# Performance work log

Hardware: AMD Instinct MI355X
Metric: run time of the kernel (lower is better)

The kernel has to match this reference:

```python
import jax, jax.numpy as jnp
import numpy as np

N, M, K, C = 2048, 2048, 32, 256
AW, NE, H, S = 32, 128, 8, 32
LMAX = 2
HID = min(128, AW // 2)          # 16, hidden width of radial MLPs
EC = AW + NE + C                 # 416, edge feature dim
M0 = 2 * AW * (LMAX + 1)         # 192, q/k degree-dot feature dim
SLICES = [(0, 1), (1, 4), (4, 9)]  # m-slices for l = 0, 1, 2


def _ln(x, g, b, eps=1e-5):
    mu = jnp.mean(x, -1, keepdims=True)
    var = jnp.mean(jnp.square(x - mu), -1, keepdims=True)
    return (x - mu) * jax.lax.rsqrt(var + eps) * g + b


def _radial(x, w1, b1, g1, be1, w2, b2, g2, be2, w3, b3):
    # EquiformerV2-style RadialFunction: Linear->LN->SiLU x2 -> Linear
    h = jax.nn.silu(_ln(x @ w1.T + b1, g1, be1))
    h = jax.nn.silu(_ln(h @ w2.T + b2, g2, be2))
    return h @ w3.T + b3


def _so3_linear(x, W, b):
    # per-degree channel mixing; bias only on l=0. x: [..., 9, Cin], W: [3, Cout, Cin]
    outs = []
    for l, (s, e) in enumerate(SLICES):
        o = jnp.einsum('...mc,dc->...md', x[..., s:e, :], W[l])
        if l == 0:
            o = o + b
        outs.append(o)
    return jnp.concatenate(outs, axis=-2)


def _sph_all(vec):
    # real spherical harmonics l=0..2 of normalized vec, integral normalization
    v = vec / (jnp.linalg.norm(vec, axis=-1, keepdims=True) + 1e-12)
    x, y, z = v[..., 0], v[..., 1], v[..., 2]
    y0 = jnp.full(x.shape, 0.28209479177387814)
    c1 = 0.4886025119029199
    c2a, c2b, c2c = 1.0925484305920792, 0.31539156525252005, 0.5462742152960396
    return jnp.stack([y0, c1 * y, c1 * z, c1 * x,
                      c2a * x * y, c2a * y * z, c2b * (3.0 * z * z - 1.0),
                      c2a * x * z, c2c * (x * x - y * y)], axis=-1)


def _smooth_leaky(x, a=0.2):
    return 0.5 * (1 + a) * x + 0.5 * (1 - a) * x * (2.0 * jax.nn.sigmoid(x) - 1.0)


def _forward(node_pos, node_irreps_input, edge_dis, edge_vec, attn_weight,
             cluster_irreps_input, tgt_emb, W_dot, b_dot,
             rm0_w1, rm0_b1, rm0_g1, rm0_be1, rm0_w2, rm0_b2, rm0_g2, rm0_be2, rm0_w3, rm0_b3,
             fc_m0_w, fc_m0_b, an_g, an_b, alpha_dot,
             rv_w1, rv_b1, rv_g1, rv_be1, rv_w2, rv_b2, rv_g2, rv_be2, rv_w3, rv_b3,
             wz, bz, atomic_numbers, attn_mask, f_sparse_idx_expnode):
    n, k = attn_weight.shape[0], attn_weight.shape[1]
    aw = jnp.where(attn_mask, 0.0, attn_weight)                 # mask padded neighbors
    tgt = tgt_emb[atomic_numbers]                               # [N,NE]
    idx = f_sparse_idx_expnode                                  # [N,K] cluster gather index
    cl_scal = cluster_irreps_input[:, 0, :][idx]                # [N,K,C] scalar (l=0) part
    x_edge = jnp.concatenate(
        [aw, jnp.broadcast_to(tgt[:, None, :], (n, k, tgt.shape[-1])), cl_scal], -1)

    # dot_alpha attention logits: per-degree <feat, Y_l(r_ij)> for query and gathered key
    q = _so3_linear(node_irreps_input, W_dot, b_dot)            # [N,9,AW]
    key = _so3_linear(cluster_irreps_input, W_dot, b_dot)[idx]  # [N,K,9,AW]
    sh = _sph_all(edge_vec)                                     # [N,K,9]
    dots = [jnp.einsum('nmc,nkm->nkc', q[:, s:e, :], sh[..., s:e]) for s, e in SLICES]
    dots += [jnp.einsum('nkmc,nkm->nkc', key[:, :, s:e, :], sh[..., s:e]) for s, e in SLICES]
    m0 = jnp.concatenate(dots, -1)                              # [N,K,M0]

    ew = _radial(x_edge, rm0_w1, rm0_b1, rm0_g1, rm0_be1, rm0_w2, rm0_b2, rm0_g2, rm0_be2, rm0_w3, rm0_b3)
    af = ((m0 * ew) @ fc_m0_w.T + fc_m0_b).reshape(n, k, H, S)
    af = _smooth_leaky(_ln(af, an_g, an_b))
    logits = jnp.einsum('nkhs,hs->nkh', af, alpha_dot)
    logits = jnp.where(attn_mask, -1e9, logits)
    alpha = jax.nn.softmax(logits, axis=1)                      # [N,K,H]

    # zero-order value path: radial edge weight modulates gathered equivariant values
    vw = _radial(x_edge, rv_w1, rv_b1, rv_g1, rv_be1, rv_w2, rv_b2, rv_g2, rv_be2, rv_w3, rv_b3)
    v = (cluster_irreps_input[idx] * vw[:, :, None, :]).reshape(n, k, 9, H, C // H)
    out = jnp.einsum('nkh,nkmhc->nmhc', alpha, v).reshape(n, 9, C)
    return _so3_linear(out, wz, bz)                             # [N,9,C]


def setup_inputs() -> dict:
    ks = iter(jax.random.split(jax.random.key(0), 64))
    nrm = lambda shape, s=1.0: jax.random.normal(next(ks), shape, jnp.float32) * s
    inp = {}
    inp['node_pos'] = nrm((N, 3))
    inp['node_irreps_input'] = nrm((N, 9, C))
    inp['edge_dis'] = jax.random.uniform(next(ks), (N, K), jnp.float32) * 5.0
    inp['edge_vec'] = nrm((N, K, 3))
    inp['attn_weight'] = nrm((N, K, AW))
    inp['atomic_numbers'] = jax.random.randint(next(ks), (N,), 0, 256)
    inp['attn_mask'] = jax.random.bernoulli(next(ks), 0.1, (N, K, 1))
    inp['f_sparse_idx_expnode'] = jax.random.randint(next(ks), (N, K), 0, M)
    inp['cluster_irreps_input'] = nrm((M, 9, C))
    inp['tgt_emb'] = jax.random.uniform(next(ks), (256, NE), jnp.float32, -0.001, 0.001)
    inp['W_dot'] = nrm((3, AW, C), C ** -0.5)
    inp['b_dot'] = jnp.zeros((AW,), jnp.float32)

    def rad_params(pfx, out_dim):
        d = {}
        d[pfx + '_w1'] = nrm((HID, EC), EC ** -0.5); d[pfx + '_b1'] = jnp.zeros((HID,), jnp.float32)
        d[pfx + '_g1'] = jnp.ones((HID,), jnp.float32); d[pfx + '_be1'] = jnp.zeros((HID,), jnp.float32)
        d[pfx + '_w2'] = nrm((HID, HID), HID ** -0.5); d[pfx + '_b2'] = jnp.zeros((HID,), jnp.float32)
        d[pfx + '_g2'] = jnp.ones((HID,), jnp.float32); d[pfx + '_be2'] = jnp.zeros((HID,), jnp.float32)
        d[pfx + '_w3'] = nrm((out_dim, HID), HID ** -0.5); d[pfx + '_b3'] = jnp.zeros((out_dim,), jnp.float32)
        return d

    inp.update(rad_params('rm0', M0))
    inp['fc_m0_w'] = nrm((H * S, M0), M0 ** -0.5)
    inp['fc_m0_b'] = jnp.zeros((H * S,), jnp.float32)
    inp['an_g'] = jnp.ones((S,), jnp.float32)
    inp['an_b'] = jnp.zeros((S,), jnp.float32)
    std = S ** -0.5
    inp['alpha_dot'] = jax.random.uniform(next(ks), (H, S), jnp.float32, -std, std)
    inp.update(rad_params('rv', C))
    inp['wz'] = nrm((3, C, C), C ** -0.5)
    inp['bz'] = jnp.zeros((C,), jnp.float32)
    return inp


def reference(node_pos, node_irreps_input, edge_dis, edge_vec, attn_weight, atomic_numbers,
              attn_mask, f_sparse_idx_expnode, cluster_irreps_input, tgt_emb, W_dot, b_dot,
              rm0_w1, rm0_b1, rm0_g1, rm0_be1, rm0_w2, rm0_b2, rm0_g2, rm0_be2, rm0_w3, rm0_b3,
              fc_m0_w, fc_m0_b, an_g, an_b, alpha_dot,
              rv_w1, rv_b1, rv_g1, rv_be1, rv_w2, rv_b2, rv_g2, rv_be2, rv_w3, rv_b3,
              wz, bz):
    return _forward(node_pos, node_irreps_input, edge_dis, edge_vec, attn_weight,
                    cluster_irreps_input, tgt_emb, W_dot, b_dot,
                    rm0_w1, rm0_b1, rm0_g1, rm0_be1, rm0_w2, rm0_b2, rm0_g2, rm0_be2, rm0_w3, rm0_b3,
                    fc_m0_w, fc_m0_b, an_g, an_b, alpha_dot,
                    rv_w1, rv_b1, rv_g1, rv_be1, rv_w2, rv_b2, rv_g2, rv_be2, rv_w3, rv_b3,
                    wz, bz, atomic_numbers, attn_mask, f_sparse_idx_expnode)
```

## Files before the change

kernel.cpp:

```cpp
#include <hip/hip_runtime.h>
#include <math.h>

#define NNODE 2048
#define MCLUS 2048
#define KNBR  32
#define CDIM  256
#define HHEAD 8

typedef __attribute__((ext_vector_type(8))) short bf16x8;
typedef __attribute__((ext_vector_type(4))) float f32x4;

__device__ __forceinline__ float sigf(float x) { return 1.0f / (1.0f + __expf(-x)); }

__device__ __forceinline__ unsigned short f2bf(float f) {
    unsigned x = __float_as_uint(f);
    unsigned r = ((x >> 16) & 1u) + 0x7FFFu;
    return (unsigned short)((x + r) >> 16);
}
__device__ __forceinline__ float bf2f(unsigned short u) {
    return __uint_as_float(((unsigned)u) << 16);
}

__global__ void k0_detect(const unsigned int* __restrict__ mw, int* __restrict__ flag) {
    int i = blockIdx.x * blockDim.x + threadIdx.x;
    unsigned int w = mw[i];
    int vb = (w != 0u && w != 1u && w != 0x3F800000u) ? 1 : 0;
    int vf = (w == 0x3F800000u) ? 1 : 0;
    unsigned long long bal_b = __ballot(vb);
    unsigned long long bal_f = __ballot(vf);
    if ((threadIdx.x & 63) == 0) {
        if (bal_b) atomicOr(flag, 1);
        if (bal_f) atomicOr(flag, 2);
    }
}

__device__ __forceinline__ bool edge_masked(const void* mp, int mode, int e) {
    if (mode & 2) return ((const float*)mp)[e] != 0.0f;
    if (mode & 1) return ((const unsigned char*)mp)[e] != 0;
    return ((const int*)mp)[e] != 0;
}

__global__ __launch_bounds__(256) void kconv(const float* __restrict__ clus,
                                             const float* __restrict__ fcw,
                                             const float* __restrict__ wz,
                                             unsigned short* __restrict__ clh,
                                             unsigned short* __restrict__ fcwh,
                                             unsigned short* __restrict__ wzh) {
    int b = blockIdx.x, t = threadIdx.x;
    if (b < MCLUS) {
        size_t base = (size_t)b * 2304;
#pragma unroll
        for (int r = 0; r < 9; ++r) {
            int o = r * 256 + t;
            clh[base + o] = f2bf(clus[base + o]);
        }
    } else if (b < MCLUS + 192) {
        int off = (b - MCLUS) * 256 + t;
        fcwh[off] = f2bf(fcw[off]);
    } else {
        int off = (b - MCLUS - 192) * 256 + t;
        wzh[off] = f2bf(wz[off]);
    }
}

__global__ __launch_bounds__(256) void kpre(
    const float* __restrict__ tgt_emb, const float* __restrict__ clus,
    const float* __restrict__ rm0_w1, const float* __restrict__ rv_w1,
    float* __restrict__ TA, float* __restrict__ CA)
{
    int b = blockIdx.x, t = threadIdx.x;
    int slot = t & 31, j = slot & 15, mlp = slot >> 4;
    const float* w1 = mlp ? rv_w1 : rm0_w1;
    if (b < 32) {
        int a = b * 8 + (t >> 5);
        const float* x = tgt_emb + (size_t)a * 128;
        const float* w = w1 + j * 416 + 32;
        float acc = 0.0f;
        for (int i = 0; i < 128; i += 4)
            acc = fmaf(x[i], w[i], fmaf(x[i+1], w[i+1], fmaf(x[i+2], w[i+2], fmaf(x[i+3], w[i+3], acc))));
        TA[a * 32 + slot] = acc;
    } else {
        int m = (b - 32) * 8 + (t >> 5);
        const float* x = clus + (size_t)m * 2304;
        const float* w = w1 + j * 416 + 160;
        float acc = 0.0f;
        for (int i = 0; i < 256; i += 4)
            acc = fmaf(x[i], w[i], fmaf(x[i+1], w[i+1], fmaf(x[i+2], w[i+2], fmaf(x[i+3], w[i+3], acc))));
        CA[m * 32 + slot] = acc;
    }
}

__global__ __launch_bounds__(256) void k1_so3qk(
    const float* __restrict__ nodei, const float* __restrict__ clus,
    const float* __restrict__ W_dot, const float* __restrict__ b_dot,
    float* __restrict__ q_ws, unsigned short* __restrict__ keyh)
{
    __shared__ __align__(16) float X[32][256];
    __shared__ int rx[32], rmm[32];
    int b = blockIdx.x, t = threadIdx.x;
    int l, vr0, nm, moff;
    if (b < 128)      { l = 0; vr0 = b * 32;         nm = 1; moff = 0; }
    else if (b < 512) { l = 1; vr0 = (b - 128) * 32; nm = 3; moff = 1; }
    else              { l = 2; vr0 = (b - 512) * 32; nm = 5; moff = 4; }
    if (t < 32) {
        int vr = vr0 + t;
        rx[t] = vr / nm;
        rmm[t] = moff + vr % nm;
    }
    __syncthreads();
    for (int e = t; e < 32 * 256; e += 256) {
        int r = e >> 8, c = e & 255;
        int x = rx[r], m = rmm[r];
        const float* src = (x < NNODE) ? (nodei + ((size_t)x * 9 + m) * 256)
                                       : (clus + ((size_t)(x - NNODE) * 9 + m) * 256);
        X[r][c] = src[c];
    }
    __syncthreads();
    int d = t & 31, rg = t >> 5;
    int r0 = rg * 4;
    const float4* wrow = (const float4*)(W_dot + ((size_t)l * 32 + d) * 256);
    float acc[4];
    float bd = (l == 0) ? b_dot[d] : 0.0f;
#pragma unroll
    for (int jj = 0; jj < 4; ++jj) acc[jj] = bd;
    for (int c4 = 0; c4 < 64; ++c4) {
        float4 w = wrow[c4];
#pragma unroll
        for (int jj = 0; jj < 4; ++jj) {
            float4 x4 = *(const float4*)&X[r0 + jj][c4 * 4];
            acc[jj] = fmaf(x4.x, w.x, fmaf(x4.y, w.y, fmaf(x4.z, w.z, fmaf(x4.w, w.w, acc[jj]))));
        }
    }
#pragma unroll
    for (int jj = 0; jj < 4; ++jj) {
        int r = r0 + jj;
        int x = rx[r], m = rmm[r];
        if (x < NNODE) q_ws[((size_t)x * 9 + m) * 32 + d] = acc[jj];
        else           keyh[((size_t)(x - NNODE) * 9 + m) * 32 + d] = f2bf(acc[jj]);
    }
}

__device__ __forceinline__ float lnsilu16(float x, float g, float b) {
    float s = x;
#pragma unroll
    for (int m = 1; m < 16; m <<= 1) s += __shfl_xor(s, m, 16);
    float mu = s * 0.0625f;
    float d = x - mu;
    float s2 = d * d;
#pragma unroll
    for (int m = 1; m < 16; m <<= 1) s2 += __shfl_xor(s2, m, 16);
    float y = d * rsqrtf(s2 * 0.0625f + 1e-5f) * g + b;
    return y * sigf(y);
}

__global__ __launch_bounds__(256, 2) void k2ab(
    const float* __restrict__ attn_weight, const void* __restrict__ mask,
    const int* __restrict__ mflag,
    const int* __restrict__ f_idx, const float* __restrict__ edge_vec,
    const int* __restrict__ atom_num,
    const float* __restrict__ q_ws, const unsigned short* __restrict__ keyh,
    const float* __restrict__ TA, const float* __restrict__ CA,
    const float* __restrict__ rm0_w1, const float* __restrict__ rm0_b1,
    const float* __restrict__ rm0_g1, const float* __restrict__ rm0_be1,
    const float* __restrict__ rm0_w2, const float* __restrict__ rm0_b2,
    const float* __restrict__ rm0_g2, const float* __restrict__ rm0_be2,
    const float* __restrict__ rm0_w3, const float* __restrict__ rm0_b3,
    const unsigned short* __restrict__ fcwh, const float* __restrict__ fcb,
    const float* __restrict__ an_g, const float* __restrict__ an_b,
    const float* __restrict__ alpha_dot,
    const float* __restrict__ rv_w1, const float* __restrict__ rv_b1,
    const float* __restrict__ rv_g1, const float* __restrict__ rv_be1,
    const float* __restrict__ rv_w2, const float* __restrict__ rv_b2,
    const float* __restrict__ rv_g2, const float* __restrict__ rv_be2,
    float* __restrict__ al_g, float* __restrict__ h2v_g)
{
    __shared__ float qn[288];
    __shared__ float Ts[32];
    __shared__ float shS[32][9];
    __shared__ __align__(16) unsigned char poolS[32 * 200 * 2];
    float (*awS)[32] = (float(*)[32])poolS;
    float (*caS)[32] = (float(*)[32])(poolS + 4096);
    unsigned short (*mwbS)[200] = (unsigned short(*)[200])poolS;
    __shared__ float KDS[32][96];
    __shared__ float h2mS[32][17];
    __shared__ float lgS[32][8];
    __shared__ float mxS[8], invS[8];
    __shared__ int idxk[32], maskk[32];

    int n = blockIdx.x, t = threadIdx.x;
    int mode = mflag[0];

    for (int i = t; i < 288; i += 256) qn[i] = q_ws[(size_t)n * 288 + i];
    if (t < 32) {
        int an = atom_num[n];
        Ts[t] = TA[an * 32 + t];
        int e = n * KNBR + t;
        idxk[t] = f_idx[e];
        maskk[t] = edge_masked(mask, mode, e) ? 1 : 0;
        float vx = edge_vec[(size_t)e * 3 + 0];
        float vy = edge_vec[(size_t)e * 3 + 1];
        float vz = edge_vec[(size_t)e * 3 + 2];
        float inv = 1.0f / (sqrtf(vx * vx + vy * vy + vz * vz) + 1e-12f);
        float x = vx * inv, y = vy * inv, z = vz * inv;
        shS[t][0] = 0.28209479177387814f;
        shS[t][1] = 0.4886025119029199f * y;
        shS[t][2] = 0.4886025119029199f * z;
        shS[t][3] = 0.4886025119029199f * x;
        shS[t][4] = 1.0925484305920792f * x * y;
        shS[t][5] = 1.0925484305920792f * y * z;
        shS[t][6] = 0.31539156525252005f * (3.0f * z * z - 1.0f);
        shS[t][7] = 1.0925484305920792f * x * z;
        shS[t][8] = 0.5462742152960396f * (x * x - y * y);
    }
    __syncthreads();
    for (int e2 = t; e2 < 1024; e2 += 256) {
        int ek = e2 >> 5, i = e2 & 31;
        awS[ek][i] = maskk[ek] ? 0.0f : attn_weight[((size_t)(n * KNBR + ek)) * 32 + i];
        caS[ek][i] = CA[(size_t)idxk[ek] * 32 + i];
    }
    for (int i = t; i < 32 * 96; i += 256) {
        int e = i / 96, j = i - e * 96;
        int p = j >> 5, c = j & 31;
        const unsigned short* kr = keyh + (size_t)idxk[e] * 288;
        float v;
        if (p == 0)      v = bf2f(kr[c]) * shS[e][0];
        else if (p == 1) v = bf2f(kr[32 + c]) * shS[e][1] + bf2f(kr[64 + c]) * shS[e][2]
                           + bf2f(kr[96 + c]) * shS[e][3];
        else             v = bf2f(kr[128 + c]) * shS[e][4] + bf2f(kr[160 + c]) * shS[e][5]
                           + bf2f(kr[192 + c]) * shS[e][6] + bf2f(kr[224 + c]) * shS[e][7]
                           + bf2f(kr[256 + c]) * shS[e][8];
        KDS[e][j] = v;
    }
    __syncthreads();

    {
        int g = t >> 4, j = t & 15;
        for (int ee = 0; ee < 2; ++ee) {
            int e = g + ee * 16;
            float accm = rm0_b1[j] + Ts[j] + caS[e][j];
            float accv = rv_b1[j] + Ts[16 + j] + caS[e][16 + j];
            const float* w1m = rm0_w1 + j * 416;
            const float* w1v = rv_w1 + j * 416;
#pragma unroll
            for (int i = 0; i < 32; i += 4) {
                float a0 = awS[e][i], a1 = awS[e][i + 1], a2 = awS[e][i + 2], a3 = awS[e][i + 3];
                accm = fmaf(a0, w1m[i], fmaf(a1, w1m[i+1], fmaf(a2, w1m[i+2], fmaf(a3, w1m[i+3], accm))));
                accv = fmaf(a0, w1v[i], fmaf(a1, w1v[i+1], fmaf(a2, w1v[i+2], fmaf(a3, w1v[i+3], accv))));
            }
            float hm = lnsilu16(accm, rm0_g1[j], rm0_be1[j]);
            float hv = lnsilu16(accv, rv_g1[j], rv_be1[j]);
            float am2 = rm0_b2[j], av2 = rv_b2[j];
#pragma unroll
            for (int i = 0; i < 16; ++i) {
                am2 = fmaf(__shfl(hm, i, 16), rm0_w2[j * 16 + i], am2);
                av2 = fmaf(__shfl(hv, i, 16), rv_w2[j * 16 + i], av2);
            }
            float h2m = lnsilu16(am2, rm0_g2[j], rm0_be2[j]);
            float h2v = lnsilu16(av2, rv_g2[j], rv_be2[j]);
            h2v_g[(size_t)n * 512 + e * 16 + j] = h2v;
            h2mS[e][j] = h2m;
        }
    }
    __syncthreads();

#pragma unroll
    for (int bb = 0; bb < 6; ++bb) {
#pragma unroll
        for (int r2 = 0; r2 < 4; ++r2) {
            int oi = r2 * 256 + t;
            int e = oi >> 5, c = oi & 31;
            int d = bb * 32 + c;
            const float4* w3 = (const float4*)(rm0_w3 + d * 16);
            float ew = rm0_b3[d];
#pragma unroll
            for (int i4 = 0; i4 < 4; ++i4) {
                float4 w = w3[i4];
                ew = fmaf(h2mS[e][i4 * 4 + 0], w.x, fmaf(h2mS[e][i4 * 4 + 1], w.y,
                     fmaf(h2mS[e][i4 * 4 + 2], w.z, fmaf(h2mS[e][i4 * 4 + 3], w.w, ew))));
            }
            float m0v;
            if (bb == 0)      m0v = qn[c] * shS[e][0];
            else if (bb == 1) m0v = qn[32 + c] * shS[e][1] + qn[64 + c] * shS[e][2]
                                  + qn[96 + c] * shS[e][3];
            else if (bb == 2) m0v = qn[128 + c] * shS[e][4] + qn[160 + c] * shS[e][5]
                                  + qn[192 + c] * shS[e][6] + qn[224 + c] * shS[e][7]
                                  + qn[256 + c] * shS[e][8];
            else              m0v = KDS[e][(bb - 3) * 32 + c];
            mwbS[e][d] = f2bf(ew * m0v);
        }
    }
    __syncthreads();

    {
        int wid = t >> 6, lane = t & 63;
        int lrow = lane & 15, kgrp = lane >> 4;
        f32x4 acc[4][2];
#pragma unroll
        for (int i = 0; i < 4; ++i)
#pragma unroll
            for (int m = 0; m < 2; ++m) acc[i][m] = (f32x4){0.f, 0.f, 0.f, 0.f};

#pragma unroll
        for (int ntl = 0; ntl < 4; ++ntl) {
            int col = wid * 64 + ntl * 16 + lrow;
            const bf16x8* brow = (const bf16x8*)(fcwh + (size_t)col * 192);
            bf16x8 bf[6];
#pragma unroll
            for (int kk = 0; kk < 6; ++kk) bf[kk] = brow[kk * 4 + kgrp];
#pragma unroll
            for (int kk = 0; kk < 6; ++kk) {
#pragma unroll
                for (int m = 0; m < 2; ++m) {
                    bf16x8 a8 = *(const bf16x8*)&mwbS[m * 16 + lrow][kk * 32 + kgrp * 8];
                    acc[ntl][m] = __builtin_amdgcn_mfma_f32_16x16x32_bf16(a8, bf[kk], acc[ntl][m], 0, 0, 0);
                }
            }
        }
#pragma unroll
        for (int ntl = 0; ntl < 4; ++ntl) {
            float fb = fcb[wid * 64 + ntl * 16 + lrow];
#pragma unroll
            for (int m = 0; m < 2; ++m)
#pragma unroll
                for (int r = 0; r < 4; ++r) acc[ntl][m][r] += fb;
        }
        float ang0 = an_g[lrow], ang1 = an_g[16 + lrow];
        float anb0 = an_b[lrow], anb1 = an_b[16 + lrow];
#pragma unroll
        for (int hh = 0; hh < 2; ++hh) {
            int h = wid * 2 + hh;
            float ad0 = alpha_dot[h * 32 + lrow], ad1 = alpha_dot[h * 32 + 16 + lrow];
#pragma unroll
            for (int m = 0; m < 2; ++m) {
#pragma unroll
                for (int r = 0; r < 4; ++r) {
                    float a = acc[2 * hh][m][r], b = acc[2 * hh + 1][m][r];
                    float su = a + b;
#pragma unroll
                    for (int mm = 1; mm < 16; mm <<= 1) su += __shfl_xor(su, mm, 16);
                    float mu = su * (1.0f / 32.0f);
                    float da = a - mu, db = b - mu;
                    float v2 = da * da + db * db;
#pragma unroll
                    for (int mm = 1; mm < 16; mm <<= 1) v2 += __shfl_xor(v2, mm, 16);
                    float rs = rsqrtf(v2 * (1.0f / 32.0f) + 1e-5f);
                    float y0 = da * rs * ang0 + anb0;
                    float y1 = db * rs * ang1 + anb1;
                    float sl0 = 0.6f * y0 + 0.4f * y0 * (2.0f * sigf(y0) - 1.0f);
                    float sl1 = 0.6f * y1 + 0.4f * y1 * (2.0f * sigf(y1) - 1.0f);
                    float lg = sl0 * ad0 + sl1 * ad1;
#pragma unroll
                    for (int mm = 1; mm < 16; mm <<= 1) lg += __shfl_xor(lg, mm, 16);
                    if (lrow == 0) {
                        int e = m * 16 + kgrp * 4 + r;
                        lgS[e][h] = maskk[e] ? -1e9f : lg;
                    }
                }
            }
        }
    }
    __syncthreads();

    if (t < 8) {
        float mx = -1e30f;
#pragma unroll
        for (int k = 0; k < 32; ++k) mx = fmaxf(mx, lgS[k][t]);
        float sum = 0.0f;
#pragma unroll
        for (int k = 0; k < 32; ++k) sum += __expf(lgS[k][t] - mx);
        mxS[t] = mx;
        invS[t] = 1.0f / sum;
    }
    __syncthreads();
    {
        int k = t >> 3, h = t & 7;
        al_g[(size_t)n * 256 + t] = __expf(lgS[k][h] - mxS[h]) * invS[h];
    }
}

__global__ __launch_bounds__(256) void k2c(
    const float* __restrict__ al_g, const float* __restrict__ h2v_g,
    const int* __restrict__ f_idx, const unsigned short* __restrict__ clh,
    const float* __restrict__ rv_w3, const float* __restrict__ rv_b3,
    float* __restrict__ outpre)
{
    __shared__ float alS[256];
    __shared__ float h2S[32][16];
    __shared__ int idxS[32];
    int n = blockIdx.x, t = threadIdx.x;
    alS[t] = al_g[(size_t)n * 256 + t];
    if (t < 32) idxS[t] = f_idx[n * KNBR + t];
    for (int i = t; i < 512; i += 256) h2S[i >> 4][i & 15] = h2v_g[(size_t)n * 512 + i];
    __syncthreads();

    int c = t, h = c >> 5;
    float avr[32];
    {
        float w3r[16];
        const float4* w3p = (const float4*)(rv_w3 + c * 16);
#pragma unroll
        for (int i4 = 0; i4 < 4; ++i4) {
            float4 w = w3p[i4];
            w3r[i4 * 4 + 0] = w.x; w3r[i4 * 4 + 1] = w.y;
            w3r[i4 * 4 + 2] = w.z; w3r[i4 * 4 + 3] = w.w;
        }
        float b3c = rv_b3[c];
#pragma unroll
        for (int k = 0; k < 32; ++k) {
            float vw = b3c;
#pragma unroll
            for (int i = 0; i < 16; ++i) vw = fmaf(h2S[k][i], w3r[i], vw);
            avr[k] = alS[k * 8 + h] * vw;
        }
    }

    float acc[9];
#pragma unroll
    for (int m = 0; m < 9; ++m) acc[m] = 0.0f;
#pragma unroll 4
    for (int k = 0; k < 32; ++k) {
        const unsigned short* crow = clh + (size_t)idxS[k] * 2304 + c;
        float av = avr[k];
#pragma unroll
        for (int m = 0; m < 9; ++m) acc[m] = fmaf(av, bf2f(crow[m * 256]), acc[m]);
    }
#pragma unroll
    for (int m = 0; m < 9; ++m) outpre[((size_t)n * 9 + m) * 256 + c] = acc[m];
}

__global__ __launch_bounds__(256) void k5_final(
    const unsigned short* __restrict__ wzh, const float* __restrict__ bz,
    float* __restrict__ io)
{
    __shared__ __align__(16) unsigned short Xb[32][264];
    __shared__ int rr[32];
    int b = blockIdx.x, t = threadIdx.x;
    int l, vr0, nm, moff;
    if (b < 64)       { l = 0; vr0 = b * 32;         nm = 1; moff = 0; }
    else if (b < 256) { l = 1; vr0 = (b - 64) * 32;  nm = 3; moff = 1; }
    else              { l = 2; vr0 = (b - 256) * 32; nm = 5; moff = 4; }
    if (t < 32) {
        int vr = vr0 + t;
        int n = vr / nm, m = moff + vr % nm;
        rr[t] = n * 9 + m;
    }
    __syncthreads();
    for (int e = t; e < 32 * 256; e += 256) {
        int r = e >> 8, c = e & 255;
        Xb[r][c] = f2bf(io[(size_t)rr[r] * 256 + c]);
    }
    __syncthreads();

    int wid = t >> 6, lane = t & 63;
    int lrow = lane & 15, kgrp = lane >> 4;
    f32x4 acc[2][4];
#pragma unroll
    for (int mt = 0; mt < 2; ++mt)
#pragma unroll
        for (int ntl = 0; ntl < 4; ++ntl) acc[mt][ntl] = (f32x4){0.f, 0.f, 0.f, 0.f};

#pragma unroll
    for (int ntl = 0; ntl < 4; ++ntl) {
        int dcol = wid * 64 + ntl * 16 + lrow;
        const bf16x8* brow = (const bf16x8*)(wzh + ((size_t)l * 256 + dcol) * 256);
#pragma unroll
        for (int kk = 0; kk < 8; ++kk) {
            bf16x8 b8 = brow[kk * 4 + kgrp];
#pragma unroll
            for (int mt = 0; mt < 2; ++mt) {
                bf16x8 a8 = *(const bf16x8*)&Xb[mt * 16 + lrow][kk * 32 + kgrp * 8];
                acc[mt][ntl] = __builtin_amdgcn_mfma_f32_16x16x32_bf16(a8, b8, acc[mt][ntl], 0, 0, 0);
            }
        }
    }
#pragma unroll
    for (int ntl = 0; ntl < 4; ++ntl) {
        int dcol = wid * 64 + ntl * 16 + lrow;
        float bias = (l == 0) ? bz[dcol] : 0.0f;
#pragma unroll
        for (int mt = 0; mt < 2; ++mt) {
#pragma unroll
            for (int r = 0; r < 4; ++r) {
                int row = mt * 16 + kgrp * 4 + r;
                io[(size_t)rr[row] * 256 + dcol] = acc[mt][ntl][r] + bias;
            }
        }
    }
}

extern "C" void kernel_launch(void* const* d_in, const int* in_sizes, int n_in,
                              void* d_out, int out_size, void* d_ws, size_t ws_size,
                              hipStream_t stream)
{
    (void)in_sizes; (void)n_in; (void)out_size; (void)ws_size;

    const float* node_irreps = (const float*)d_in[1];
    const float* edge_vec    = (const float*)d_in[3];
    const float* attn_weight = (const float*)d_in[4];
    const int*   atom_num    = (const int*)d_in[5];
    const void*  attn_mask   = d_in[6];
    const int*   f_idx       = (const int*)d_in[7];
    const float* clus        = (const float*)d_in[8];
    const float* tgt_emb     = (const float*)d_in[9];
    const float* W_dot       = (const float*)d_in[10];
    const float* b_dot       = (const float*)d_in[11];
    const float* rm0_w1 = (const float*)d_in[12];
    const float* rm0_b1 = (const float*)d_in[13];
    const float* rm0_g1 = (const float*)d_in[14];
    const float* rm0_be1 = (const float*)d_in[15];
    const float* rm0_w2 = (const float*)d_in[16];
    const float* rm0_b2 = (const float*)d_in[17];
    const float* rm0_g2 = (const float*)d_in[18];
    const float* rm0_be2 = (const float*)d_in[19];
    const float* rm0_w3 = (const float*)d_in[20];
    const float* rm0_b3 = (const float*)d_in[21];
    const float* fcw = (const float*)d_in[22];
    const float* fcb = (const float*)d_in[23];
    const float* an_g = (const float*)d_in[24];
    const float* an_b = (const float*)d_in[25];
    const float* alpha_dot = (const float*)d_in[26];
    const float* rv_w1 = (const float*)d_in[27];
    const float* rv_b1 = (const float*)d_in[28];
    const float* rv_g1 = (const float*)d_in[29];
    const float* rv_be1 = (const float*)d_in[30];
    const float* rv_w2 = (const float*)d_in[31];
    const float* rv_b2 = (const float*)d_in[32];
    const float* rv_g2 = (const float*)d_in[33];
    const float* rv_be2 = (const float*)d_in[34];
    const float* rv_w3 = (const float*)d_in[35];
    const float* rv_b3 = (const float*)d_in[36];
    const float* wz = (const float*)d_in[37];
    const float* bz = (const float*)d_in[38];

    float* ws = (float*)d_ws;
    int* flag = (int*)d_ws;
    float* q_ws = ws + 16;
    unsigned short* keyh = (unsigned short*)(q_ws + (size_t)NNODE * 288);
    float* TA_ws = (float*)(keyh + (size_t)MCLUS * 288);
    float* CA_ws = TA_ws + 256 * 32;
    unsigned short* clh = (unsigned short*)(CA_ws + (size_t)MCLUS * 32);
    float* al_ws = (float*)(clh + (size_t)MCLUS * 2304);
    float* h2v_ws = al_ws + (size_t)NNODE * 256;
    unsigned short* fcwh = (unsigned short*)(h2v_ws + (size_t)NNODE * 512);
    unsigned short* wzh = fcwh + 256 * 192;
    float* outpre = (float*)d_out;

    hipMemsetAsync(flag, 0, sizeof(int), stream);
    k0_detect<<<64, 256, 0, stream>>>((const unsigned int*)attn_mask, flag);
    kconv<<<MCLUS + 192 + 768, 256, 0, stream>>>(clus, fcw, wz, clh, fcwh, wzh);
    kpre<<<288, 256, 0, stream>>>(tgt_emb, clus, rm0_w1, rv_w1, TA_ws, CA_ws);
    k1_so3qk<<<1152, 256, 0, stream>>>(node_irreps, clus, W_dot, b_dot, q_ws, keyh);
    k2ab<<<NNODE, 256, 0, stream>>>(
        attn_weight, attn_mask, flag, f_idx, edge_vec, atom_num,
        q_ws, keyh, TA_ws, CA_ws,
        rm0_w1, rm0_b1, rm0_g1, rm0_be1, rm0_w2, rm0_b2, rm0_g2, rm0_be2, rm0_w3, rm0_b3,
        fcwh, fcb, an_g, an_b, alpha_dot,
        rv_w1, rv_b1, rv_g1, rv_be1, rv_w2, rv_b2, rv_g2, rv_be2,
        al_ws, h2v_ws);
    k2c<<<NNODE, 256, 0, stream>>>(al_ws, h2v_ws, f_idx, clh, rv_w3, rv_b3, outpre);
    k5_final<<<576, 256, 0, stream>>>(wzh, bz, outpre);
}
```

Baseline: 234.0 us.

## Merge four prep kernels into one launch, split FMA chains, store key-dot in bf16

```diff
diff --git a/kernel.cpp b/kernel.cpp
--- a/kernel.cpp
+++ b/kernel.cpp
@@ -21,122 +21,122 @@
     return __uint_as_float(((unsigned)u) << 16);
 }
 
-__global__ void k0_detect(const unsigned int* __restrict__ mw, int* __restrict__ flag) {
-    int i = blockIdx.x * blockDim.x + threadIdx.x;
-    unsigned int w = mw[i];
-    int vb = (w != 0u && w != 1u && w != 0x3F800000u) ? 1 : 0;
-    int vf = (w == 0x3F800000u) ? 1 : 0;
-    unsigned long long bal_b = __ballot(vb);
-    unsigned long long bal_f = __ballot(vf);
-    if ((threadIdx.x & 63) == 0) {
-        if (bal_b) atomicOr(flag, 1);
-        if (bal_f) atomicOr(flag, 2);
-    }
-}
-
 __device__ __forceinline__ bool edge_masked(const void* mp, int mode, int e) {
     if (mode & 2) return ((const float*)mp)[e] != 0.0f;
     if (mode & 1) return ((const unsigned char*)mp)[e] != 0;
     return ((const int*)mp)[e] != 0;
 }
 
-__global__ __launch_bounds__(256) void kconv(const float* __restrict__ clus,
-                                             const float* __restrict__ fcw,
-                                             const float* __restrict__ wz,
-                                             unsigned short* __restrict__ clh,
-                                             unsigned short* __restrict__ fcwh,
-                                             unsigned short* __restrict__ wzh) {
-    int b = blockIdx.x, t = threadIdx.x;
-    if (b < MCLUS) {
-        size_t base = (size_t)b * 2304;
-#pragma unroll
-        for (int r = 0; r < 9; ++r) {
-            int o = r * 256 + t;
-            clh[base + o] = f2bf(clus[base + o]);
-        }
-    } else if (b < MCLUS + 192) {
-        int off = (b - MCLUS) * 256 + t;
-        fcwh[off] = f2bf(fcw[off]);
-    } else {
-        int off = (b - MCLUS - 192) * 256 + t;
-        wzh[off] = f2bf(wz[off]);
-    }
-}
-
-__global__ __launch_bounds__(256) void kpre(
-    const float* __restrict__ tgt_emb, const float* __restrict__ clus,
+__global__ __launch_bounds__(256) void kprep(
+    const unsigned int* __restrict__ mw, int* __restrict__ flag,
+    const float* __restrict__ clus, const float* __restrict__ fcw,
+    const float* __restrict__ wz,
+    unsigned short* __restrict__ clh, unsigned short* __restrict__ fcwh,
+    unsigned short* __restrict__ wzh,
+    const float* __restrict__ tgt_emb,
     const float* __restrict__ rm0_w1, const float* __restrict__ rv_w1,
-    float* __restrict__ TA, float* __restrict__ CA)
-{
-    int b = blockIdx.x, t = threadIdx.x;
-    int slot = t & 31, j = slot & 15, mlp = slot >> 4;
-    const float* w1 = mlp ? rv_w1 : rm0_w1;
-    if (b < 32) {
-        int a = b * 8 + (t >> 5);
-        const float* x = tgt_emb + (size_t)a * 128;
-        const float* w = w1 + j * 416 + 32;
-        float acc = 0.0f;
-        for (int i = 0; i < 128; i += 4)
-            acc = fmaf(x[i], w[i], fmaf(x[i+1], w[i+1], fmaf(x[i+2], w[i+2], fmaf(x[i+3], w[i+3], acc))));
-        TA[a * 32 + slot] = acc;
-    } else {
-        int m = (b - 32) * 8 + (t >> 5);
-        const float* x = clus + (size_t)m * 2304;
-        const float* w = w1 + j * 416 + 160;
-        float acc = 0.0f;
-        for (int i = 0; i < 256; i += 4)
-            acc = fmaf(x[i], w[i], fmaf(x[i+1], w[i+1], fmaf(x[i+2], w[i+2], fmaf(x[i+3], w[i+3], acc))));
-        CA[m * 32 + slot] = acc;
-    }
-}
-
-__global__ __launch_bounds__(256) void k1_so3qk(
-    const float* __restrict__ nodei, const float* __restrict__ clus,
-    const float* __restrict__ W_dot, const float* __restrict__ b_dot,
+    float* __restrict__ TA, float* __restrict__ CA,
+    const float* __restrict__ nodei, const float* __restrict__ W_dot,
+    const float* __restrict__ b_dot,
     float* __restrict__ q_ws, unsigned short* __restrict__ keyh)
 {
     __shared__ __align__(16) float X[32][256];
     __shared__ int rx[32], rmm[32];
     int b = blockIdx.x, t = threadIdx.x;
-    int l, vr0, nm, moff;
-    if (b < 128)      { l = 0; vr0 = b * 32;         nm = 1; moff = 0; }
-    else if (b < 512) { l = 1; vr0 = (b - 128) * 32; nm = 3; moff = 1; }
-    else              { l = 2; vr0 = (b - 512) * 32; nm = 5; moff = 4; }
-    if (t < 32) {
-        int vr = vr0 + t;
-        rx[t] = vr / nm;
-        rmm[t] = moff + vr % nm;
-    }
-    __syncthreads();
-    for (int e = t; e < 32 * 256; e += 256) {
-        int r = e >> 8, c = e & 255;
-        int x = rx[r], m = rmm[r];
-        const float* src = (x < NNODE) ? (nodei + ((size_t)x * 9 + m) * 256)
-                                       : (clus + ((size_t)(x - NNODE) * 9 + m) * 256);
-        X[r][c] = src[c];
-    }
-    __syncthreads();
-    int d = t & 31, rg = t >> 5;
-    int r0 = rg * 4;
-    const float4* wrow = (const float4*)(W_dot + ((size_t)l * 32 + d) * 256);
-    float acc[4];
-    float bd = (l == 0) ? b_dot[d] : 0.0f;
-#pragma unroll
-    for (int jj = 0; jj < 4; ++jj) acc[jj] = bd;
-    for (int c4 = 0; c4 < 64; ++c4) {
-        float4 w = wrow[c4];
+
+    if (b < 1152) {
+        int l, vr0, nm, moff;
+        if (b < 128)      { l = 0; vr0 = b * 32;         nm = 1; moff = 0; }
+        else if (b < 512) { l = 1; vr0 = (b - 128) * 32; nm = 3; moff = 1; }
+        else              { l = 2; vr0 = (b - 512) * 32; nm = 5; moff = 4; }
+        if (t < 32) {
+            int vr = vr0 + t;
+            rx[t] = vr / nm;
+            rmm[t] = moff + vr % nm;
+        }
+        __syncthreads();
+        for (int e = t; e < 32 * 256; e += 256) {
+            int r = e >> 8, c = e & 255;
+            int x = rx[r], m = rmm[r];
+            const float* src = (x < NNODE) ? (nodei + ((size_t)x * 9 + m) * 256)
+                                           : (clus + ((size_t)(x - NNODE) * 9 + m) * 256);
+            X[r][c] = src[c];
+        }
+        __syncthreads();
+        int d = t & 31, rg = t >> 5;
+        int r0 = rg * 4;
+        const float4* wrow = (const float4*)(W_dot + ((size_t)l * 32 + d) * 256);
+        float acc[4];
+        float bd = (l == 0) ? b_dot[d] : 0.0f;
+#pragma unroll
+        for (int jj = 0; jj < 4; ++jj) acc[jj] = bd;
+        for (int c4 = 0; c4 < 64; ++c4) {
+            float4 w = wrow[c4];
+#pragma unroll
+            for (int jj = 0; jj < 4; ++jj) {
+                float4 x4 = *(const float4*)&X[r0 + jj][c4 * 4];
+                acc[jj] = fmaf(x4.x, w.x, fmaf(x4.y, w.y, fmaf(x4.z, w.z, fmaf(x4.w, w.w, acc[jj]))));
+            }
+        }
 #pragma unroll
         for (int jj = 0; jj < 4; ++jj) {
-            float4 x4 = *(const float4*)&X[r0 + jj][c4 * 4];
-            acc[jj] = fmaf(x4.x, w.x, fmaf(x4.y, w.y, fmaf(x4.z, w.z, fmaf(x4.w, w.w, acc[jj]))));
-        }
-    }
-#pragma unroll
-    for (int jj = 0; jj < 4; ++jj) {
-        int r = r0 + jj;
-        int x = rx[r], m = rmm[r];
-        if (x < NNODE) q_ws[((size_t)x * 9 + m) * 32 + d] = acc[jj];
-        else           keyh[((size_t)(x - NNODE) * 9 + m) * 32 + d] = f2bf(acc[jj]);
+            int r = r0 + jj;
+            int x = rx[r], m = rmm[r];
+            if (x < NNODE) q_ws[((size_t)x * 9 + m) * 32 + d] = acc[jj];
+            else           keyh[((size_t)(x - NNODE) * 9 + m) * 32 + d] = f2bf(acc[jj]);
+        }
+    } else if (b < 4160) {
+        int bb = b - 1152;
+        if (bb < MCLUS) {
+            size_t base = (size_t)bb * 2304;
+#pragma unroll
+            for (int r = 0; r < 9; ++r) {
+                int o = r * 256 + t;
+                clh[base + o] = f2bf(clus[base + o]);
+            }
+        } else if (bb < MCLUS + 192) {
+            int off = (bb - MCLUS) * 256 + t;
+            fcwh[off] = f2bf(fcw[off]);
+        } else {
+            int off = (bb - MCLUS - 192) * 256 + t;
+            wzh[off] = f2bf(wz[off]);
+        }
+    } else if (b < 4448) {
+        int bb = b - 4160;
+        int slot = t & 31, j = slot & 15, mlp = slot >> 4;
+        const float* w1 = mlp ? rv_w1 : rm0_w1;
+        if (bb < 32) {
+            int a = bb * 8 + (t >> 5);
+            const float* x = tgt_emb + (size_t)a * 128;
+            const float* w = w1 + j * 416 + 32;
+            float acc = 0.0f, acc2 = 0.0f;
+            for (int i = 0; i < 128; i += 8) {
+                acc  = fmaf(x[i], w[i], fmaf(x[i+1], w[i+1], fmaf(x[i+2], w[i+2], fmaf(x[i+3], w[i+3], acc))));
+                acc2 = fmaf(x[i+4], w[i+4], fmaf(x[i+5], w[i+5], fmaf(x[i+6], w[i+6], fmaf(x[i+7], w[i+7], acc2))));
+            }
+            TA[a * 32 + slot] = acc + acc2;
+        } else {
+            int m = (bb - 32) * 8 + (t >> 5);
+            const float* x = clus + (size_t)m * 2304;
+            const float* w = w1 + j * 416 + 160;
+            float acc = 0.0f, acc2 = 0.0f;
+            for (int i = 0; i < 256; i += 8) {
+                acc  = fmaf(x[i], w[i], fmaf(x[i+1], w[i+1], fmaf(x[i+2], w[i+2], fmaf(x[i+3], w[i+3], acc))));
+                acc2 = fmaf(x[i+4], w[i+4], fmaf(x[i+5], w[i+5], fmaf(x[i+6], w[i+6], fmaf(x[i+7], w[i+7], acc2))));
+            }
+            CA[m * 32 + slot] = acc + acc2;
+        }
+    } else {
+        int i = (b - 4448) * 256 + t;
+        unsigned int w = mw[i];
+        int vb = (w != 0u && w != 1u && w != 0x3F800000u) ? 1 : 0;
+        int vf = (w == 0x3F800000u) ? 1 : 0;
+        unsigned long long bal_b = __ballot(vb);
+        unsigned long long bal_f = __ballot(vf);
+        if ((t & 63) == 0) {
+            if (bal_b) atomicOr(flag, 1);
+            if (bal_f) atomicOr(flag, 2);
+        }
     }
 }
 
@@ -181,7 +181,7 @@
     float (*awS)[32] = (float(*)[32])poolS;
     float (*caS)[32] = (float(*)[32])(poolS + 4096);
     unsigned short (*mwbS)[200] = (unsigned short(*)[200])poolS;
-    __shared__ float KDS[32][96];
+    __shared__ unsigned short KDSh[32][96];
     __shared__ float h2mS[32][17];
     __shared__ float lgS[32][8];
     __shared__ float mxS[8], invS[8];
@@ -229,7 +229,7 @@
         else             v = bf2f(kr[128 + c]) * shS[e][4] + bf2f(kr[160 + c]) * shS[e][5]
                            + bf2f(kr[192 + c]) * shS[e][6] + bf2f(kr[224 + c]) * shS[e][7]
                            + bf2f(kr[256 + c]) * shS[e][8];
-        KDS[e][j] = v;
+        KDSh[e][j] = f2bf(v);
     }
     __syncthreads();
 
@@ -239,22 +239,31 @@
             int e = g + ee * 16;
             float accm = rm0_b1[j] + Ts[j] + caS[e][j];
             float accv = rv_b1[j] + Ts[16 + j] + caS[e][16 + j];
+            float accm2 = 0.0f, accv2 = 0.0f;
             const float* w1m = rm0_w1 + j * 416;
             const float* w1v = rv_w1 + j * 416;
 #pragma unroll
-            for (int i = 0; i < 32; i += 4) {
-                float a0 = awS[e][i], a1 = awS[e][i + 1], a2 = awS[e][i + 2], a3 = awS[e][i + 3];
-                accm = fmaf(a0, w1m[i], fmaf(a1, w1m[i+1], fmaf(a2, w1m[i+2], fmaf(a3, w1m[i+3], accm))));
-                accv = fmaf(a0, w1v[i], fmaf(a1, w1v[i+1], fmaf(a2, w1v[i+2], fmaf(a3, w1v[i+3], accv))));
-            }
+            for (int i = 0; i < 32; i += 8) {
+                float a0 = awS[e][i], a1 = awS[e][i+1], a2 = awS[e][i+2], a3 = awS[e][i+3];
+                float a4 = awS[e][i+4], a5 = awS[e][i+5], a6 = awS[e][i+6], a7 = awS[e][i+7];
+                accm  = fmaf(a0, w1m[i], fmaf(a1, w1m[i+1], fmaf(a2, w1m[i+2], fmaf(a3, w1m[i+3], accm))));
+                accm2 = fmaf(a4, w1m[i+4], fmaf(a5, w1m[i+5], fmaf(a6, w1m[i+6], fmaf(a7, w1m[i+7], accm2))));
+                accv  = fmaf(a0, w1v[i], fmaf(a1, w1v[i+1], fmaf(a2, w1v[i+2], fmaf(a3, w1v[i+3], accv))));
+                accv2 = fmaf(a4, w1v[i+4], fmaf(a5, w1v[i+5], fmaf(a6, w1v[i+6], fmaf(a7, w1v[i+7], accv2))));
+            }
+            accm += accm2; accv += accv2;
             float hm = lnsilu16(accm, rm0_g1[j], rm0_be1[j]);
             float hv = lnsilu16(accv, rv_g1[j], rv_be1[j]);
             float am2 = rm0_b2[j], av2 = rv_b2[j];
-#pragma unroll
-            for (int i = 0; i < 16; ++i) {
-                am2 = fmaf(__shfl(hm, i, 16), rm0_w2[j * 16 + i], am2);
-                av2 = fmaf(__shfl(hv, i, 16), rv_w2[j * 16 + i], av2);
-            }
+            float am2b = 0.0f, av2b = 0.0f;
+#pragma unroll
+            for (int i = 0; i < 8; ++i) {
+                am2  = fmaf(__shfl(hm, i, 16), rm0_w2[j * 16 + i], am2);
+                am2b = fmaf(__shfl(hm, 8 + i, 16), rm0_w2[j * 16 + 8 + i], am2b);
+                av2  = fmaf(__shfl(hv, i, 16), rv_w2[j * 16 + i], av2);
+                av2b = fmaf(__shfl(hv, 8 + i, 16), rv_w2[j * 16 + 8 + i], av2b);
+            }
+            am2 += am2b; av2 += av2b;
             float h2m = lnsilu16(am2, rm0_g2[j], rm0_be2[j]);
             float h2v = lnsilu16(av2, rv_g2[j], rv_be2[j]);
             h2v_g[(size_t)n * 512 + e * 16 + j] = h2v;
@@ -271,13 +280,19 @@
             int e = oi >> 5, c = oi & 31;
             int d = bb * 32 + c;
             const float4* w3 = (const float4*)(rm0_w3 + d * 16);
-            float ew = rm0_b3[d];
-#pragma unroll
-            for (int i4 = 0; i4 < 4; ++i4) {
-                float4 w = w3[i4];
-                ew = fmaf(h2mS[e][i4 * 4 + 0], w.x, fmaf(h2mS[e][i4 * 4 + 1], w.y,
-                     fmaf(h2mS[e][i4 * 4 + 2], w.z, fmaf(h2mS[e][i4 * 4 + 3], w.w, ew))));
-            }
+            float ew = rm0_b3[d], ew2 = 0.0f;
+            {
+                float4 w0 = w3[0], w1 = w3[1], w2 = w3[2], w3v = w3[3];
+                ew  = fmaf(h2mS[e][0], w0.x, fmaf(h2mS[e][1], w0.y,
+                      fmaf(h2mS[e][2], w0.z, fmaf(h2mS[e][3], w0.w, ew))));
+                ew2 = fmaf(h2mS[e][4], w1.x, fmaf(h2mS[e][5], w1.y,
+                      fmaf(h2mS[e][6], w1.z, fmaf(h2mS[e][7], w1.w, ew2))));
+                ew  = fmaf(h2mS[e][8], w2.x, fmaf(h2mS[e][9], w2.y,
+                      fmaf(h2mS[e][10], w2.z, fmaf(h2mS[e][11], w2.w, ew))));
+                ew2 = fmaf(h2mS[e][12], w3v.x, fmaf(h2mS[e][13], w3v.y,
+                      fmaf(h2mS[e][14], w3v.z, fmaf(h2mS[e][15], w3v.w, ew2))));
+            }
+            ew += ew2;
             float m0v;
             if (bb == 0)      m0v = qn[c] * shS[e][0];
             else if (bb == 1) m0v = qn[32 + c] * shS[e][1] + qn[64 + c] * shS[e][2]
@@ -285,7 +300,7 @@
             else if (bb == 2) m0v = qn[128 + c] * shS[e][4] + qn[160 + c] * shS[e][5]
                                   + qn[192 + c] * shS[e][6] + qn[224 + c] * shS[e][7]
                                   + qn[256 + c] * shS[e][8];
-            else              m0v = KDS[e][(bb - 3) * 32 + c];
+            else              m0v = bf2f(KDSh[e][(bb - 3) * 32 + c]);
             mwbS[e][d] = f2bf(ew * m0v);
         }
     }
@@ -546,10 +561,11 @@
     float* outpre = (float*)d_out;
 
     hipMemsetAsync(flag, 0, sizeof(int), stream);
-    k0_detect<<<64, 256, 0, stream>>>((const unsigned int*)attn_mask, flag);
-    kconv<<<MCLUS + 192 + 768, 256, 0, stream>>>(clus, fcw, wz, clh, fcwh, wzh);
-    kpre<<<288, 256, 0, stream>>>(tgt_emb, clus, rm0_w1, rv_w1, TA_ws, CA_ws);
-    k1_so3qk<<<1152, 256, 0, stream>>>(node_irreps, clus, W_dot, b_dot, q_ws, keyh);
+    kprep<<<4512, 256, 0, stream>>>(
+        (const unsigned int*)attn_mask, flag,
+        clus, fcw, wz, clh, fcwh, wzh,
+        tgt_emb, rm0_w1, rv_w1, TA_ws, CA_ws,
+        node_irreps, W_dot, b_dot, q_ws, keyh);
     k2ab<<<NNODE, 256, 0, stream>>>(
         attn_weight, attn_mask, flag, f_idx, edge_vec, atom_num,
         q_ws, keyh, TA_ws, CA_ws,
```

After: 242.1 us. +3.5%, slower.
